# Performance work log

Hardware: AMD Instinct MI355X
Metric: run time of the kernel (lower is better)

## Reference

```python
import jax, jax.numpy as jnp
import numpy as np

N_NODES = 50000
N_EDGES = 800000
D_IN, D_HID, D_OUT = 128, 128, 64


def setup_inputs() -> dict:
    key = jax.random.key(0)
    ks = jax.random.split(key, 8)
    x = jax.random.normal(ks[0], (N_NODES, D_IN), dtype=jnp.float32)
    edge_index = jax.random.randint(ks[1], (2, N_EDGES), 0, N_NODES, dtype=jnp.int64)
    s1 = 1.0 / np.sqrt(D_IN)
    s2 = 1.0 / np.sqrt(D_HID)
    # PyG SAGEConv: out = lin_l(mean_aggr(x_j)) + lin_r(x_root); bias lives in lin_l
    Wl1 = jax.random.uniform(ks[2], (D_HID, D_IN), jnp.float32, -s1, s1)
    bl1 = jnp.zeros((D_HID,), jnp.float32)
    Wr1 = jax.random.uniform(ks[3], (D_HID, D_IN), jnp.float32, -s1, s1)
    Wl2 = jax.random.uniform(ks[4], (D_OUT, D_HID), jnp.float32, -s2, s2)
    bl2 = jnp.zeros((D_OUT,), jnp.float32)
    Wr2 = jax.random.uniform(ks[5], (D_OUT, D_HID), jnp.float32, -s2, s2)
    return {"x": x, "edge_index": edge_index, "Wl1": Wl1, "bl1": bl1, "Wr1": Wr1,
            "Wl2": Wl2, "bl2": bl2, "Wr2": Wr2}


def _sage_conv(x, src, dst, Wl, bl, Wr):
    # mean aggregation of source-node features onto destination nodes
    msg = x[src]                                              # [E, d]
    agg = jax.ops.segment_sum(msg, dst, num_segments=N_NODES)  # [N, d]
    cnt = jax.ops.segment_sum(jnp.ones((src.shape[0],), x.dtype), dst,
                              num_segments=N_NODES)            # [N]
    mean = agg / jnp.maximum(cnt, 1.0)[:, None]
    return mean @ Wl.T + bl + x @ Wr.T


def reference(x, edge_index, Wl1, bl1, Wr1, Wl2, bl2, Wr2):
    src, dst = edge_index[0], edge_index[1]
    h = jax.nn.relu(_sage_conv(x, src, dst, Wl1, bl1, Wr1))
    h = jax.nn.relu(_sage_conv(h, src, dst, Wl2, bl2, Wr2))
    return jax.nn.log_softmax(h, axis=-1)
```

## Files before the change

### kernel.cpp

```cpp
#include <hip/hip_runtime.h>
#include <cstdint>
#include <cstddef>

#define N_NODES 50000
#define N_EDGES 800000
#define ROWS_PAD 50048
#define ZROW 50000
#define BUCKET_CAP 64

#define CNT_POISON 0xAAAAAAAAu
__device__ __forceinline__ unsigned cnt_decode(unsigned raw) {
  return raw > 0x40000000u ? raw - CNT_POISON : raw;
}

typedef _Float16 f16;
typedef _Float16 f16x2 __attribute__((ext_vector_type(2)));
typedef _Float16 f16x8 __attribute__((ext_vector_type(8)));
typedef float f32x2 __attribute__((ext_vector_type(2)));
typedef float f32x4 __attribute__((ext_vector_type(4)));
typedef float fx4 __attribute__((ext_vector_type(4)));
typedef unsigned int u32x2 __attribute__((ext_vector_type(2)));
typedef unsigned short us4 __attribute__((ext_vector_type(4)));


#define NRANGE 8
#define NCHUNK 200
#define CHUNK_E (N_EDGES / NCHUNK)
#define NB_FILL (NCHUNK * NRANGE)
#define NB_CX 3125
#define NB_CW 192
#define RANGE_SZ (N_NODES / NRANGE)

__global__ __launch_bounds__(256) void preprocess_kernel(
    const int* __restrict__ edge, unsigned* __restrict__ cnt, unsigned short* __restrict__ bucket,
    const float* __restrict__ x, f16* __restrict__ X16, unsigned char* __restrict__ X8,
    unsigned char* __restrict__ H8,
    const float* __restrict__ Wl1, const float* __restrict__ Wr1,
    const float* __restrict__ Wl2, const float* __restrict__ Wr2,
    f16* __restrict__ Wc1, f16* __restrict__ Wc2) {
  const int b = blockIdx.x;
  const int tid = threadIdx.x;
  if (b < NB_FILL) {
    const int cg = b >> 6, r = (b >> 3) & 7, cl = b & 7;
    const int chunk = cg * 8 + cl;
    const int lo = r * RANGE_SZ, hi = lo + RANGE_SZ;
    const int e0 = chunk * CHUNK_E;
    #pragma unroll
    for (int i = 0; i < 16; ++i) {
      const int e = e0 + tid + i * 256;
      if (e < e0 + CHUNK_E) {
        const int dst = edge[N_EDGES + e];
        if (dst >= lo && dst < hi) {
          const int src = edge[e];
          const unsigned pos = cnt_decode(atomicAdd(&cnt[dst], 1u));
          if (pos < BUCKET_CAP) bucket[(size_t)dst * BUCKET_CAP + pos] = (unsigned short)src;
        }
      }
    }
  } else if (b < NB_FILL + NB_CX) {
    const int idx = (b - NB_FILL) * 256 + tid;
    const int row = idx >> 4, c8 = idx & 15;
    const fx4 v0 = __builtin_nontemporal_load(
        reinterpret_cast<const fx4*>(x + (size_t)row * 128 + c8 * 8));
    const fx4 v1 = __builtin_nontemporal_load(
        reinterpret_cast<const fx4*>(x + (size_t)row * 128 + c8 * 8 + 4));
    f16x8 o;
    o[0] = (f16)v0[0]; o[1] = (f16)v0[1]; o[2] = (f16)v0[2]; o[3] = (f16)v0[3];
    o[4] = (f16)v1[0]; o[5] = (f16)v1[1]; o[6] = (f16)v1[2]; o[7] = (f16)v1[3];
    *reinterpret_cast<f16x8*>(X16 + (size_t)row * 128 + c8 * 8) = o;
    u32x2 p;
    int w = __builtin_amdgcn_cvt_pk_fp8_f32(v0[0], v0[1], 0, false);
    w = __builtin_amdgcn_cvt_pk_fp8_f32(v0[2], v0[3], w, true);
    p[0] = (unsigned int)w;
    w = __builtin_amdgcn_cvt_pk_fp8_f32(v1[0], v1[1], 0, false);
    w = __builtin_amdgcn_cvt_pk_fp8_f32(v1[2], v1[3], w, true);
    p[1] = (unsigned int)w;
    *reinterpret_cast<u32x2*>(X8 + (size_t)row * 128 + c8 * 8) = p;
  } else if (b < NB_FILL + NB_CX + NB_CW) {
    const int idx = (b - NB_FILL - NB_CX) * 256 + tid;
    if (idx < 128 * 256) {
      const int n = idx >> 8, k = idx & 255;
      Wc1[idx] = (f16)((k < 128) ? Wl1[n * 128 + k] : Wr1[n * 128 + (k - 128)]);
    } else {
      const int j = idx - 128 * 256;
      const int n = j >> 8, k = j & 255;
      Wc2[j] = (f16)((k < 128) ? Wl2[n * 128 + k] : Wr2[n * 128 + (k - 128)]);
    }
  } else {
    if (tid < 32)
      reinterpret_cast<unsigned int*>(X8 + (size_t)ZROW * 128)[tid] = 0u;
    else if (tid < 64)
      reinterpret_cast<unsigned int*>(H8 + (size_t)ZROW * 128)[tid - 32] = 0u;
  }
}


__device__ __forceinline__ void aggregate_to_lds(
    const unsigned char* __restrict__ F8, const unsigned* __restrict__ cnt,
    const unsigned short* __restrict__ bucket,
    f16 (*M)[136], int wid, int lane) {
  const int quad = lane >> 4, l16 = lane & 15;
  const int nb0 = blockIdx.x * 32 + wid * 8;
  const int dv = (lane < 8) ? (int)cnt_decode(cnt[nb0 + lane]) : 0;
  us4 b4g[2];
  #pragma unroll
  for (int g = 0; g < 2; ++g)
    b4g[g] = __builtin_nontemporal_load(reinterpret_cast<const us4*>(
        bucket + (size_t)(nb0 + g * 4 + quad) * BUCKET_CAP + l16 * 4));
  const unsigned char* Fsrc = F8 + l16 * 8;
  #pragma unroll 1
  for (int g = 0; g < 2; ++g) {
    const int dq = __shfl(dv, g * 4 + quad, 64);
    const int dqc = min(dq, BUCKET_CAP);
    int md = max(max(__shfl(dv, g * 4 + 0, 64), __shfl(dv, g * 4 + 1, 64)),
                 max(__shfl(dv, g * 4 + 2, 64), __shfl(dv, g * 4 + 3, 64)));
    md = min(md, BUCKET_CAP);
    const us4 b4 = b4g[g];
    float acc[8];
    #pragma unroll
    for (int c = 0; c < 8; ++c) acc[c] = 0.f;
    for (int j = 0; j < md; j += 16) {
      u32x2 v[16];
      #pragma unroll
      for (int k = 0; k < 16; ++k) {
        const int slot = j + k;
        const int idx = __shfl((int)b4[k & 3], quad * 16 + (slot >> 2), 64);
        const int row = (slot < dqc) ? idx : ZROW;
        v[k] = *reinterpret_cast<const u32x2*>(Fsrc + (size_t)row * 128);
      }
      #pragma unroll
      for (int k = 0; k < 16; ++k) {
        const f32x2 f0 = __builtin_amdgcn_cvt_pk_f32_fp8((int)v[k][0], false);
        const f32x2 f1 = __builtin_amdgcn_cvt_pk_f32_fp8((int)v[k][0], true);
        const f32x2 f2 = __builtin_amdgcn_cvt_pk_f32_fp8((int)v[k][1], false);
        const f32x2 f3 = __builtin_amdgcn_cvt_pk_f32_fp8((int)v[k][1], true);
        acc[0] += f0[0]; acc[1] += f0[1]; acc[2] += f1[0]; acc[3] += f1[1];
        acc[4] += f2[0]; acc[5] += f2[1]; acc[6] += f3[0]; acc[7] += f3[1];
      }
    }
    const float inv = 1.0f / (float)(dq > 0 ? dq : 1);
    f16x8 o;
    #pragma unroll
    for (int c = 0; c < 8; ++c) o[c] = (f16)(acc[c] * inv);
    *reinterpret_cast<f16x8*>(&M[wid * 8 + g * 4 + quad][l16 * 8]) = o;
  }
}


__global__ __launch_bounds__(256, 4) void layer1_kernel(
    const f16* __restrict__ X16, const unsigned char* __restrict__ X8,
    const unsigned* __restrict__ cnt, const unsigned short* __restrict__ bucket,
    const f16* __restrict__ Wc, const float* __restrict__ bias,
    f16* __restrict__ H16, unsigned char* __restrict__ H8) {
  __shared__ f16 M[32][136];
  const int wid = threadIdx.x >> 6, lane = threadIdx.x & 63;
  const int quad = lane >> 4, l16 = lane & 15;
  const int rhalf = wid & 1, nhalf = wid >> 1;
  const int row0 = blockIdx.x * 32 + rhalf * 16;
  const f16* Xrow = X16 + (size_t)(row0 + l16) * 128 + quad * 8;
  f16x8 rr[4];
  #pragma unroll
  for (int s2 = 0; s2 < 4; ++s2)
    rr[s2] = __builtin_nontemporal_load(reinterpret_cast<const f16x8*>(Xrow + s2 * 32));
  aggregate_to_lds(X8, cnt, bucket, M, wid, lane);
  __syncthreads();
  f32x4 acc[4];
  #pragma unroll
  for (int t = 0; t < 4; ++t) acc[t] = (f32x4){0.f, 0.f, 0.f, 0.f};
  const f16x8* Wb = reinterpret_cast<const f16x8*>(Wc) + quad;
  #pragma unroll
  for (int s = 0; s < 8; ++s) {
    const f16x8 a = (s < 4)
        ? *reinterpret_cast<const f16x8*>(&M[rhalf * 16 + l16][quad * 8 + s * 32])
        : rr[s - 4];
    #pragma unroll
    for (int t = 0; t < 4; ++t) {
      const int u = nhalf * 4 + t;
      const f16x8 bb = Wb[(u * 16 + l16) * 32 + s * 4];
      acc[t] = __builtin_amdgcn_mfma_f32_16x16x32_f16(a, bb, acc[t], 0, 0, 0);
    }
  }
  #pragma unroll
  for (int t = 0; t < 4; ++t) {
    const int col = (nhalf * 4 + t) * 16 + l16;
    const float bv = bias[col];
    #pragma unroll
    for (int r = 0; r < 4; ++r) {
      const int row = row0 + quad * 4 + r;
      if (row < N_NODES) {
        const float vv = fmaxf(acc[t][r] + bv, 0.f);
        H16[(size_t)row * 128 + col] = (f16)vv;
        const int p = __builtin_amdgcn_cvt_pk_fp8_f32(vv, vv, 0, false);
        H8[(size_t)row * 128 + col] = (unsigned char)(p & 0xFF);
      }
    }
  }
}


__global__ __launch_bounds__(256, 4) void layer2_kernel(
    const f16* __restrict__ H16, const unsigned char* __restrict__ H8,
    const unsigned* __restrict__ cnt, const unsigned short* __restrict__ bucket,
    const f16* __restrict__ Wc, const float* __restrict__ bias,
    float* __restrict__ out) {
  __shared__ f16 M[32][136];
  __shared__ float PM[4][16], PS[4][16];
  const int wid = threadIdx.x >> 6, lane = threadIdx.x & 63;
  const int quad = lane >> 4, l16 = lane & 15;
  const int rhalf = wid & 1, nhalf = wid >> 1;
  const int row0 = blockIdx.x * 32 + rhalf * 16;
  const f16* Hrow = H16 + (size_t)(row0 + l16) * 128 + quad * 8;
  f16x8 rr[4];
  #pragma unroll
  for (int s2 = 0; s2 < 4; ++s2)
    rr[s2] = __builtin_nontemporal_load(reinterpret_cast<const f16x8*>(Hrow + s2 * 32));
  aggregate_to_lds(H8, cnt, bucket, M, wid, lane);
  __syncthreads();
  f32x4 acc[2];
  #pragma unroll
  for (int t = 0; t < 2; ++t) acc[t] = (f32x4){0.f, 0.f, 0.f, 0.f};
  const f16x8* Wb = reinterpret_cast<const f16x8*>(Wc) + quad;
  #pragma unroll
  for (int s = 0; s < 8; ++s) {
    const f16x8 a = (s < 4)
        ? *reinterpret_cast<const f16x8*>(&M[rhalf * 16 + l16][quad * 8 + s * 32])
        : rr[s - 4];
    #pragma unroll
    for (int t = 0; t < 2; ++t) {
      const int u = nhalf * 2 + t;
      const f16x8 bb = Wb[(u * 16 + l16) * 32 + s * 4];
      acc[t] = __builtin_amdgcn_mfma_f32_16x16x32_f16(a, bb, acc[t], 0, 0, 0);
    }
  }
  float bv[2];
  #pragma unroll
  for (int t = 0; t < 2; ++t) bv[t] = bias[(nhalf * 2 + t) * 16 + l16];
  float v[4][2], pm[4], ps[4];
  #pragma unroll
  for (int r = 0; r < 4; ++r) {
    #pragma unroll
    for (int t = 0; t < 2; ++t) v[r][t] = fmaxf(acc[t][r] + bv[t], 0.f);
    float m = fmaxf(v[r][0], v[r][1]);
    #pragma unroll
    for (int off = 1; off < 16; off <<= 1) m = fmaxf(m, __shfl_xor(m, off, 64));
    float s = __expf(v[r][0] - m) + __expf(v[r][1] - m);
    #pragma unroll
    for (int off = 1; off < 16; off <<= 1) s += __shfl_xor(s, off, 64);
    pm[r] = m;
    ps[r] = s;
  }
  if (l16 == 0) {
    #pragma unroll
    for (int r = 0; r < 4; ++r) {
      PM[wid][quad * 4 + r] = pm[r];
      PS[wid][quad * 4 + r] = ps[r];
    }
  }
  __syncthreads();
  #pragma unroll
  for (int r = 0; r < 4; ++r) {
    const float m2 = PM[wid ^ 2][quad * 4 + r];
    const float s2 = PS[wid ^ 2][quad * 4 + r];
    const float mt = fmaxf(pm[r], m2);
    const float st = ps[r] * __expf(pm[r] - mt) + s2 * __expf(m2 - mt);
    const float ls = mt + __logf(st);
    const int row = row0 + quad * 4 + r;
    if (row < N_NODES) {
      #pragma unroll
      for (int t = 0; t < 2; ++t)
        __builtin_nontemporal_store(
            v[r][t] - ls, out + (size_t)row * 64 + (nhalf * 2 + t) * 16 + l16);
    }
  }
}


extern "C" void kernel_launch(void* const* d_in, const int* in_sizes, int n_in,
                              void* d_out, int out_size, void* d_ws, size_t ws_size,
                              hipStream_t stream) {
  const float* x   = (const float*)d_in[0];
  const int* edge  = (const int*)d_in[1];
  const float* Wl1 = (const float*)d_in[2];
  const float* bl1 = (const float*)d_in[3];
  const float* Wr1 = (const float*)d_in[4];
  const float* Wl2 = (const float*)d_in[5];
  const float* bl2 = (const float*)d_in[6];
  const float* Wr2 = (const float*)d_in[7];
  float* out = (float*)d_out;

  char* ws = (char*)d_ws;
  size_t off = 0;
  auto alloc = [&](size_t bytes) -> char* {
    char* p = ws + off;
    off = (off + bytes + 255) & ~(size_t)255;
    return p;
  };
  unsigned* cnt          = (unsigned*)alloc((size_t)ROWS_PAD * 4);
  unsigned short* bucket = (unsigned short*)alloc((size_t)ROWS_PAD * BUCKET_CAP * 2);
  f16* X16           = (f16*)alloc((size_t)ROWS_PAD * 128 * 2);
  f16* H16           = (f16*)alloc((size_t)ROWS_PAD * 128 * 2);
  unsigned char* X8  = (unsigned char*)alloc((size_t)ROWS_PAD * 128);
  unsigned char* H8  = (unsigned char*)alloc((size_t)ROWS_PAD * 128);
  f16* Wc1           = (f16*)alloc((size_t)128 * 256 * 2);
  f16* Wc2           = (f16*)alloc((size_t)64 * 256 * 2);


  preprocess_kernel<<<NB_FILL + NB_CX + NB_CW + 1, 256, 0, stream>>>(
      edge, cnt, bucket, x, X16, X8, H8, Wl1, Wr1, Wl2, Wr2, Wc1, Wc2);

  layer1_kernel<<<ROWS_PAD / 32, 256, 0, stream>>>(X16, X8, cnt, bucket, Wc1, bl1, H16, H8);
  layer2_kernel<<<ROWS_PAD / 32, 256, 0, stream>>>(H16, H8, cnt, bucket, Wc2, bl2, out);
}
```

Before: 209.1 us.

## Software-pipeline neighbor gathers across both node groups in aggregation

Rewrites the neighbor aggregation so the two 4-node groups per wave are processed together. Gathers for the next 16-slot chunk are issued while the current chunk is decoded, so more loads are in flight and gather latency is hidden. Both groups now loop to the maximum degree over all 8 nodes instead of per group, which can add padded zero-row loads. The self-row loads are moved after the aggregation call and register use roughly doubles, which may lower occupancy.

```diff
diff --git a/kernel.cpp b/kernel.cpp
--- a/kernel.cpp
+++ b/kernel.cpp
@@ -102,48 +102,63 @@
   const int quad = lane >> 4, l16 = lane & 15;
   const int nb0 = blockIdx.x * 32 + wid * 8;
   const int dv = (lane < 8) ? (int)cnt_decode(cnt[nb0 + lane]) : 0;
-  us4 b4g[2];
-  #pragma unroll
-  for (int g = 0; g < 2; ++g)
-    b4g[g] = __builtin_nontemporal_load(reinterpret_cast<const us4*>(
-        bucket + (size_t)(nb0 + g * 4 + quad) * BUCKET_CAP + l16 * 4));
+  const us4 b40 = __builtin_nontemporal_load(reinterpret_cast<const us4*>(
+      bucket + (size_t)(nb0 + quad) * BUCKET_CAP + l16 * 4));
+  const us4 b41 = __builtin_nontemporal_load(reinterpret_cast<const us4*>(
+      bucket + (size_t)(nb0 + 4 + quad) * BUCKET_CAP + l16 * 4));
   const unsigned char* Fsrc = F8 + l16 * 8;
+  const int dq0 = __shfl(dv, quad, 64);
+  const int dq1 = __shfl(dv, 4 + quad, 64);
+  const int dqc0 = min(dq0, BUCKET_CAP), dqc1 = min(dq1, BUCKET_CAP);
+  int md = 0;
+  #pragma unroll
+  for (int n = 0; n < 8; ++n) md = max(md, __shfl(dv, n, 64));
+  md = min(md, BUCKET_CAP);
+
+  float acc0[8], acc1[8];
+  #pragma unroll
+  for (int c = 0; c < 8; ++c) { acc0[c] = 0.f; acc1[c] = 0.f; }
+  u32x2 v0[16], v1[16];
+
+#define AGG_ISSUE(vv, b4x, dqcx, jj)                                          \
+  _Pragma("unroll") for (int k = 0; k < 16; ++k) {                            \
+    const int slot = (jj) + k;  \
+    const int idx = __shfl((int)(b4x)[k & 3], quad * 16 + (slot >> 2), 64);   \
+    const int row = (slot < (dqcx)) ? idx : ZROW;    \
+    (vv)[k] = *reinterpret_cast<const u32x2*>(Fsrc + (size_t)row * 128);      \
+  }
+#define AGG_DECODE(vv, accx)                                                  \
+  _Pragma("unroll") for (int k = 0; k < 16; ++k) {                            \
+    const f32x2 f0 = __builtin_amdgcn_cvt_pk_f32_fp8((int)(vv)[k][0], false); \
+    const f32x2 f1 = __builtin_amdgcn_cvt_pk_f32_fp8((int)(vv)[k][0], true);  \
+    const f32x2 f2 = __builtin_amdgcn_cvt_pk_f32_fp8((int)(vv)[k][1], false); \
+    const f32x2 f3 = __builtin_amdgcn_cvt_pk_f32_fp8((int)(vv)[k][1], true);  \
+    (accx)[0] += f0[0]; (accx)[1] += f0[1]; (accx)[2] += f1[0]; (accx)[3] += f1[1]; \
+    (accx)[4] += f2[0]; (accx)[5] += f2[1]; (accx)[6] += f3[0]; (accx)[7] += f3[1]; \
+  }
+
+  AGG_ISSUE(v0, b40, dqc0, 0)
+  AGG_ISSUE(v1, b41, dqc1, 0)
   #pragma unroll 1
-  for (int g = 0; g < 2; ++g) {
-    const int dq = __shfl(dv, g * 4 + quad, 64);
-    const int dqc = min(dq, BUCKET_CAP);
-    int md = max(max(__shfl(dv, g * 4 + 0, 64), __shfl(dv, g * 4 + 1, 64)),
-                 max(__shfl(dv, g * 4 + 2, 64), __shfl(dv, g * 4 + 3, 64)));
-    md = min(md, BUCKET_CAP);
-    const us4 b4 = b4g[g];
-    float acc[8];
-    #pragma unroll
-    for (int c = 0; c < 8; ++c) acc[c] = 0.f;
-    for (int j = 0; j < md; j += 16) {
-      u32x2 v[16];
-      #pragma unroll
-      for (int k = 0; k < 16; ++k) {
-        const int slot = j + k;
-        const int idx = __shfl((int)b4[k & 3], quad * 16 + (slot >> 2), 64);
-        const int row = (slot < dqc) ? idx : ZROW;
-        v[k] = *reinterpret_cast<const u32x2*>(Fsrc + (size_t)row * 128);
-      }
-      #pragma unroll
-      for (int k = 0; k < 16; ++k) {
-        const f32x2 f0 = __builtin_amdgcn_cvt_pk_f32_fp8((int)v[k][0], false);
-        const f32x2 f1 = __builtin_amdgcn_cvt_pk_f32_fp8((int)v[k][0], true);
-        const f32x2 f2 = __builtin_amdgcn_cvt_pk_f32_fp8((int)v[k][1], false);
-        const f32x2 f3 = __builtin_amdgcn_cvt_pk_f32_fp8((int)v[k][1], true);
-        acc[0] += f0[0]; acc[1] += f0[1]; acc[2] += f1[0]; acc[3] += f1[1];
-        acc[4] += f2[0]; acc[5] += f2[1]; acc[6] += f3[0]; acc[7] += f3[1];
-      }
-    }
-    const float inv = 1.0f / (float)(dq > 0 ? dq : 1);
-    f16x8 o;
-    #pragma unroll
-    for (int c = 0; c < 8; ++c) o[c] = (f16)(acc[c] * inv);
-    *reinterpret_cast<f16x8*>(&M[wid * 8 + g * 4 + quad][l16 * 8]) = o;
-  }
+  for (int j = 0; j < md; j += 16) {
+    AGG_DECODE(v0, acc0)
+    if (j + 16 < md) { AGG_ISSUE(v0, b40, dqc0, j + 16) }
+    AGG_DECODE(v1, acc1)
+    if (j + 16 < md) { AGG_ISSUE(v1, b41, dqc1, j + 16) }
+  }
+#undef AGG_ISSUE
+#undef AGG_DECODE
+
+  const float inv0 = 1.0f / (float)(dq0 > 0 ? dq0 : 1);
+  const float inv1 = 1.0f / (float)(dq1 > 0 ? dq1 : 1);
+  f16x8 o0, o1;
+  #pragma unroll
+  for (int c = 0; c < 8; ++c) {
+    o0[c] = (f16)(acc0[c] * inv0);
+    o1[c] = (f16)(acc1[c] * inv1);
+  }
+  *reinterpret_cast<f16x8*>(&M[wid * 8 + quad][l16 * 8]) = o0;
+  *reinterpret_cast<f16x8*>(&M[wid * 8 + 4 + quad][l16 * 8]) = o1;
 }
 
 
@@ -157,12 +172,12 @@
   const int quad = lane >> 4, l16 = lane & 15;
   const int rhalf = wid & 1, nhalf = wid >> 1;
   const int row0 = blockIdx.x * 32 + rhalf * 16;
+  aggregate_to_lds(X8, cnt, bucket, M, wid, lane);
   const f16* Xrow = X16 + (size_t)(row0 + l16) * 128 + quad * 8;
   f16x8 rr[4];
   #pragma unroll
   for (int s2 = 0; s2 < 4; ++s2)
     rr[s2] = __builtin_nontemporal_load(reinterpret_cast<const f16x8*>(Xrow + s2 * 32));
-  aggregate_to_lds(X8, cnt, bucket, M, wid, lane);
   __syncthreads();
   f32x4 acc[4];
   #pragma unroll
@@ -209,12 +224,12 @@
   const int quad = lane >> 4, l16 = lane & 15;
   const int rhalf = wid & 1, nhalf = wid >> 1;
   const int row0 = blockIdx.x * 32 + rhalf * 16;
+  aggregate_to_lds(H8, cnt, bucket, M, wid, lane);
   const f16* Hrow = H16 + (size_t)(row0 + l16) * 128 + quad * 8;
   f16x8 rr[4];
   #pragma unroll
   for (int s2 = 0; s2 < 4; ++s2)
     rr[s2] = __builtin_nontemporal_load(reinterpret_cast<const f16x8*>(Hrow + s2 * 32));
-  aggregate_to_lds(H8, cnt, bucket, M, wid, lane);
   __syncthreads();
   f32x4 acc[2];
   #pragma unroll
```

Result: slower. 285.3 us (+36.4%).

## Split fp8 feature tables into two 64-column halves for gather locality

Applied to the files above, without the earlier changes.

Stores the fp8 node features (X8, H8) as two separate 64-byte-per-row arrays instead of one 128-byte array. The aggregation gathers each half in its own pass, with two lane groups covering alternate neighbor slots, then combines the partial sums with a cross-lane xor shuffle. Each pass touches a table half the size, which should raise cache hit rates for the random gathers. The cost is twice as many passes over the neighbor list and an extra shuffle reduction.

```diff
diff --git a/kernel.cpp b/kernel.cpp
--- a/kernel.cpp
+++ b/kernel.cpp
@@ -14,7 +14,6 @@
 }
 
 typedef _Float16 f16;
-typedef _Float16 f16x2 __attribute__((ext_vector_type(2)));
 typedef _Float16 f16x8 __attribute__((ext_vector_type(8)));
 typedef float f32x2 __attribute__((ext_vector_type(2)));
 typedef float f32x4 __attribute__((ext_vector_type(4)));
@@ -33,8 +32,9 @@
 
 __global__ __launch_bounds__(256) void preprocess_kernel(
     const int* __restrict__ edge, unsigned* __restrict__ cnt, unsigned short* __restrict__ bucket,
-    const float* __restrict__ x, f16* __restrict__ X16, unsigned char* __restrict__ X8,
-    unsigned char* __restrict__ H8,
+    const float* __restrict__ x, f16* __restrict__ X16,
+    unsigned char* __restrict__ X8a, unsigned char* __restrict__ X8b,
+    unsigned char* __restrict__ H8a, unsigned char* __restrict__ H8b,
     const float* __restrict__ Wl1, const float* __restrict__ Wr1,
     const float* __restrict__ Wl2, const float* __restrict__ Wr2,
     f16* __restrict__ Wc1, f16* __restrict__ Wc2) {
@@ -75,7 +75,9 @@
     w = __builtin_amdgcn_cvt_pk_fp8_f32(v1[0], v1[1], 0, false);
     w = __builtin_amdgcn_cvt_pk_fp8_f32(v1[2], v1[3], w, true);
     p[1] = (unsigned int)w;
-    *reinterpret_cast<u32x2*>(X8 + (size_t)row * 128 + c8 * 8) = p;
+    unsigned char* dst8 = (c8 < 8) ? (X8a + (size_t)row * 64 + c8 * 8)
+                                   : (X8b + (size_t)row * 64 + (c8 - 8) * 8);
+    *reinterpret_cast<u32x2*>(dst8) = p;
   } else if (b < NB_FILL + NB_CX + NB_CW) {
     const int idx = (b - NB_FILL - NB_CX) * 256 + tid;
     if (idx < 128 * 256) {
@@ -87,19 +89,24 @@
       Wc2[j] = (f16)((k < 128) ? Wl2[n * 128 + k] : Wr2[n * 128 + (k - 128)]);
     }
   } else {
-    if (tid < 32)
-      reinterpret_cast<unsigned int*>(X8 + (size_t)ZROW * 128)[tid] = 0u;
+    if (tid < 16)
+      reinterpret_cast<unsigned int*>(X8a + (size_t)ZROW * 64)[tid] = 0u;
+    else if (tid < 32)
+      reinterpret_cast<unsigned int*>(X8b + (size_t)ZROW * 64)[tid - 16] = 0u;
+    else if (tid < 48)
+      reinterpret_cast<unsigned int*>(H8a + (size_t)ZROW * 64)[tid - 32] = 0u;
     else if (tid < 64)
-      reinterpret_cast<unsigned int*>(H8 + (size_t)ZROW * 128)[tid - 32] = 0u;
+      reinterpret_cast<unsigned int*>(H8b + (size_t)ZROW * 64)[tid - 48] = 0u;
   }
 }
 
 
 __device__ __forceinline__ void aggregate_to_lds(
-    const unsigned char* __restrict__ F8, const unsigned* __restrict__ cnt,
-    const unsigned short* __restrict__ bucket,
+    const unsigned char* __restrict__ F8a, const unsigned char* __restrict__ F8b,
+    const unsigned* __restrict__ cnt, const unsigned short* __restrict__ bucket,
     f16 (*M)[136], int wid, int lane) {
   const int quad = lane >> 4, l16 = lane & 15;
+  const int half8 = l16 >> 3, l8 = l16 & 7;
   const int nb0 = blockIdx.x * 32 + wid * 8;
   const int dv = (lane < 8) ? (int)cnt_decode(cnt[nb0 + lane]) : 0;
   us4 b4g[2];
@@ -107,7 +114,6 @@
   for (int g = 0; g < 2; ++g)
     b4g[g] = __builtin_nontemporal_load(reinterpret_cast<const us4*>(
         bucket + (size_t)(nb0 + g * 4 + quad) * BUCKET_CAP + l16 * 4));
-  const unsigned char* Fsrc = F8 + l16 * 8;
   #pragma unroll 1
   for (int g = 0; g < 2; ++g) {
     const int dq = __shfl(dv, g * 4 + quad, 64);
@@ -116,42 +122,51 @@
                  max(__shfl(dv, g * 4 + 2, 64), __shfl(dv, g * 4 + 3, 64)));
     md = min(md, BUCKET_CAP);
     const us4 b4 = b4g[g];
-    float acc[8];
-    #pragma unroll
-    for (int c = 0; c < 8; ++c) acc[c] = 0.f;
-    for (int j = 0; j < md; j += 16) {
-      u32x2 v[16];
+    const float inv = 1.0f / (float)(dq > 0 ? dq : 1);
+    #pragma unroll 1
+    for (int p = 0; p < 2; ++p) {
+      const unsigned char* Fsrc = (p == 0 ? F8a : F8b) + l8 * 8;
+      float acc[8];
       #pragma unroll
-      for (int k = 0; k < 16; ++k) {
-        const int slot = j + k;
-        const int idx = __shfl((int)b4[k & 3], quad * 16 + (slot >> 2), 64);
-        const int row = (slot < dqc) ? idx : ZROW;
-        v[k] = *reinterpret_cast<const u32x2*>(Fsrc + (size_t)row * 128);
+      for (int c = 0; c < 8; ++c) acc[c] = 0.f;
+      for (int j = 0; j < md; j += 32) {
+        u32x2 v[16];
+        #pragma unroll
+        for (int k = 0; k < 16; ++k) {
+          const int slot = j + k + half8 * 16;
+          const int idx = __shfl((int)b4[k & 3],
+                                 quad * 16 + ((j + k) >> 2) + half8 * 4, 64);
+          const int row = (slot < dqc) ? idx : ZROW;
+          v[k] = *reinterpret_cast<const u32x2*>(Fsrc + (size_t)row * 64);
+        }
+        #pragma unroll
+        for (int k = 0; k < 16; ++k) {
+          const f32x2 f0 = __builtin_amdgcn_cvt_pk_f32_fp8((int)v[k][0], false);
+          const f32x2 f1 = __builtin_amdgcn_cvt_pk_f32_fp8((int)v[k][0], true);
+          const f32x2 f2 = __builtin_amdgcn_cvt_pk_f32_fp8((int)v[k][1], false);
+          const f32x2 f3 = __builtin_amdgcn_cvt_pk_f32_fp8((int)v[k][1], true);
+          acc[0] += f0[0]; acc[1] += f0[1]; acc[2] += f1[0]; acc[3] += f1[1];
+          acc[4] += f2[0]; acc[5] += f2[1]; acc[6] += f3[0]; acc[7] += f3[1];
+        }
       }
       #pragma unroll
-      for (int k = 0; k < 16; ++k) {
-        const f32x2 f0 = __builtin_amdgcn_cvt_pk_f32_fp8((int)v[k][0], false);
-        const f32x2 f1 = __builtin_amdgcn_cvt_pk_f32_fp8((int)v[k][0], true);
-        const f32x2 f2 = __builtin_amdgcn_cvt_pk_f32_fp8((int)v[k][1], false);
-        const f32x2 f3 = __builtin_amdgcn_cvt_pk_f32_fp8((int)v[k][1], true);
-        acc[0] += f0[0]; acc[1] += f0[1]; acc[2] += f1[0]; acc[3] += f1[1];
-        acc[4] += f2[0]; acc[5] += f2[1]; acc[6] += f3[0]; acc[7] += f3[1];
-      }
-    }
-    const float inv = 1.0f / (float)(dq > 0 ? dq : 1);
-    f16x8 o;
-    #pragma unroll
-    for (int c = 0; c < 8; ++c) o[c] = (f16)(acc[c] * inv);
-    *reinterpret_cast<f16x8*>(&M[wid * 8 + g * 4 + quad][l16 * 8]) = o;
+      for (int c = 0; c < 8; ++c) acc[c] += __shfl_xor(acc[c], 8, 64);
+      f16x8 o;
+      #pragma unroll
+      for (int c = 0; c < 8; ++c) o[c] = (f16)(acc[c] * inv);
+      *reinterpret_cast<f16x8*>(&M[wid * 8 + g * 4 + quad][p * 64 + l8 * 8]) = o;
+    }
   }
 }
 
 
 __global__ __launch_bounds__(256, 4) void layer1_kernel(
-    const f16* __restrict__ X16, const unsigned char* __restrict__ X8,
+    const f16* __restrict__ X16,
+    const unsigned char* __restrict__ X8a, const unsigned char* __restrict__ X8b,
     const unsigned* __restrict__ cnt, const unsigned short* __restrict__ bucket,
     const f16* __restrict__ Wc, const float* __restrict__ bias,
-    f16* __restrict__ H16, unsigned char* __restrict__ H8) {
+    f16* __restrict__ H16,
+    unsigned char* __restrict__ H8a, unsigned char* __restrict__ H8b) {
   __shared__ f16 M[32][136];
   const int wid = threadIdx.x >> 6, lane = threadIdx.x & 63;
   const int quad = lane >> 4, l16 = lane & 15;
@@ -162,7 +177,7 @@
   #pragma unroll
   for (int s2 = 0; s2 < 4; ++s2)
     rr[s2] = __builtin_nontemporal_load(reinterpret_cast<const f16x8*>(Xrow + s2 * 32));
-  aggregate_to_lds(X8, cnt, bucket, M, wid, lane);
+  aggregate_to_lds(X8a, X8b, cnt, bucket, M, wid, lane);
   __syncthreads();
   f32x4 acc[4];
   #pragma unroll
@@ -182,8 +197,11 @@
   }
   #pragma unroll
   for (int t = 0; t < 4; ++t) {
-    const int col = (nhalf * 4 + t) * 16 + l16;
+    const int u = nhalf * 4 + t;
+    const int col = u * 16 + l16;
     const float bv = bias[col];
+    unsigned char* H8t = (u < 4) ? H8a : H8b;
+    const int colh = col & 63;
     #pragma unroll
     for (int r = 0; r < 4; ++r) {
       const int row = row0 + quad * 4 + r;
@@ -191,7 +209,7 @@
         const float vv = fmaxf(acc[t][r] + bv, 0.f);
         H16[(size_t)row * 128 + col] = (f16)vv;
         const int p = __builtin_amdgcn_cvt_pk_fp8_f32(vv, vv, 0, false);
-        H8[(size_t)row * 128 + col] = (unsigned char)(p & 0xFF);
+        H8t[(size_t)row * 64 + colh] = (unsigned char)(p & 0xFF);
       }
     }
   }
@@ -199,7 +217,8 @@
 
 
 __global__ __launch_bounds__(256, 4) void layer2_kernel(
-    const f16* __restrict__ H16, const unsigned char* __restrict__ H8,
+    const f16* __restrict__ H16,
+    const unsigned char* __restrict__ H8a, const unsigned char* __restrict__ H8b,
     const unsigned* __restrict__ cnt, const unsigned short* __restrict__ bucket,
     const f16* __restrict__ Wc, const float* __restrict__ bias,
     float* __restrict__ out) {
@@ -214,7 +233,7 @@
   #pragma unroll
   for (int s2 = 0; s2 < 4; ++s2)
     rr[s2] = __builtin_nontemporal_load(reinterpret_cast<const f16x8*>(Hrow + s2 * 32));
-  aggregate_to_lds(H8, cnt, bucket, M, wid, lane);
+  aggregate_to_lds(H8a, H8b, cnt, bucket, M, wid, lane);
   __syncthreads();
   f32x4 acc[2];
   #pragma unroll
@@ -299,15 +318,19 @@
   unsigned short* bucket = (unsigned short*)alloc((size_t)ROWS_PAD * BUCKET_CAP * 2);
   f16* X16           = (f16*)alloc((size_t)ROWS_PAD * 128 * 2);
   f16* H16           = (f16*)alloc((size_t)ROWS_PAD * 128 * 2);
-  unsigned char* X8  = (unsigned char*)alloc((size_t)ROWS_PAD * 128);
-  unsigned char* H8  = (unsigned char*)alloc((size_t)ROWS_PAD * 128);
+  unsigned char* X8a = (unsigned char*)alloc((size_t)ROWS_PAD * 64);
+  unsigned char* X8b = (unsigned char*)alloc((size_t)ROWS_PAD * 64);
+  unsigned char* H8a = (unsigned char*)alloc((size_t)ROWS_PAD * 64);
+  unsigned char* H8b = (unsigned char*)alloc((size_t)ROWS_PAD * 64);
   f16* Wc1           = (f16*)alloc((size_t)128 * 256 * 2);
   f16* Wc2           = (f16*)alloc((size_t)64 * 256 * 2);
 
 
   preprocess_kernel<<<NB_FILL + NB_CX + NB_CW + 1, 256, 0, stream>>>(
-      edge, cnt, bucket, x, X16, X8, H8, Wl1, Wr1, Wl2, Wr2, Wc1, Wc2);
-
-  layer1_kernel<<<ROWS_PAD / 32, 256, 0, stream>>>(X16, X8, cnt, bucket, Wc1, bl1, H16, H8);
-  layer2_kernel<<<ROWS_PAD / 32, 256, 0, stream>>>(H16, H8, cnt, bucket, Wc2, bl2, out);
-}
+      edge, cnt, bucket, x, X16, X8a, X8b, H8a, H8b, Wl1, Wr1, Wl2, Wr2, Wc1, Wc2);
+
+  layer1_kernel<<<ROWS_PAD / 32, 256, 0, stream>>>(
+      X16, X8a, X8b, cnt, bucket, Wc1, bl1, H16, H8a, H8b);
+  layer2_kernel<<<ROWS_PAD / 32, 256, 0, stream>>>(
+      H16, H8a, H8b, cnt, bucket, Wc2, bl2, out);
+}
```

After: 210.9 us. About the same (+0.9%).

## Apply layer-2 linear transforms before aggregation to shrink gathered features

Applied to the files above, without the earlier changes.

Uses the linearity of mean aggregation to compute H·Wl2ᵀ and H·Wr2ᵀ inside the layer-1 kernel, which adds a second MFMA stage on the hidden tile held in LDS. Layer 2 then gathers 64-wide FP8 projected rows instead of 128-wide hidden rows, and its GEMM is replaced by an add, bias, ReLU and log-softmax. This halves the gather traffic of the second aggregation and removes the H16/H8 round trip. In exchange layer 1 does more compute, and quantising the projected values to FP8 changes the numerical error profile.

```diff
diff --git a/kernel.cpp b/kernel.cpp
--- a/kernel.cpp
+++ b/kernel.cpp
@@ -14,7 +14,6 @@
 }
 
 typedef _Float16 f16;
-typedef _Float16 f16x2 __attribute__((ext_vector_type(2)));
 typedef _Float16 f16x8 __attribute__((ext_vector_type(8)));
 typedef float f32x2 __attribute__((ext_vector_type(2)));
 typedef float f32x4 __attribute__((ext_vector_type(4)));
@@ -34,10 +33,10 @@
 __global__ __launch_bounds__(256) void preprocess_kernel(
     const int* __restrict__ edge, unsigned* __restrict__ cnt, unsigned short* __restrict__ bucket,
     const float* __restrict__ x, f16* __restrict__ X16, unsigned char* __restrict__ X8,
-    unsigned char* __restrict__ H8,
+    unsigned char* __restrict__ Hp8,
     const float* __restrict__ Wl1, const float* __restrict__ Wr1,
     const float* __restrict__ Wl2, const float* __restrict__ Wr2,
-    f16* __restrict__ Wc1, f16* __restrict__ Wc2) {
+    f16* __restrict__ Wc1, f16* __restrict__ Wc2p) {
   const int b = blockIdx.x;
   const int tid = threadIdx.x;
   if (b < NB_FILL) {
@@ -83,14 +82,14 @@
       Wc1[idx] = (f16)((k < 128) ? Wl1[n * 128 + k] : Wr1[n * 128 + (k - 128)]);
     } else {
       const int j = idx - 128 * 256;
-      const int n = j >> 8, k = j & 255;
-      Wc2[j] = (f16)((k < 128) ? Wl2[n * 128 + k] : Wr2[n * 128 + (k - 128)]);
+      const int n = j >> 7, k = j & 127;
+      Wc2p[j] = (f16)((n < 64) ? Wl2[n * 128 + k] : Wr2[(n - 64) * 128 + k]);
     }
   } else {
     if (tid < 32)
       reinterpret_cast<unsigned int*>(X8 + (size_t)ZROW * 128)[tid] = 0u;
-    else if (tid < 64)
-      reinterpret_cast<unsigned int*>(H8 + (size_t)ZROW * 128)[tid - 32] = 0u;
+    else if (tid < 48)
+      reinterpret_cast<unsigned int*>(Hp8 + (size_t)ZROW * 64)[tid - 32] = 0u;
   }
 }
 
@@ -151,8 +150,10 @@
     const f16* __restrict__ X16, const unsigned char* __restrict__ X8,
     const unsigned* __restrict__ cnt, const unsigned short* __restrict__ bucket,
     const f16* __restrict__ Wc, const float* __restrict__ bias,
-    f16* __restrict__ H16, unsigned char* __restrict__ H8) {
+    const f16* __restrict__ Wc2p,
+    unsigned char* __restrict__ Hp8, f16* __restrict__ R2f) {
   __shared__ f16 M[32][136];
+  __shared__ f16 HT[32][136];
   const int wid = threadIdx.x >> 6, lane = threadIdx.x & 63;
   const int quad = lane >> 4, l16 = lane & 15;
   const int rhalf = wid & 1, nhalf = wid >> 1;
@@ -186,12 +187,40 @@
     const float bv = bias[col];
     #pragma unroll
     for (int r = 0; r < 4; ++r) {
+      const int rl = rhalf * 16 + quad * 4 + r;
+      HT[rl][col] = (f16)fmaxf(acc[t][r] + bv, 0.f);
+    }
+  }
+  __syncthreads();
+  f32x4 acc2[4];
+  #pragma unroll
+  for (int t = 0; t < 4; ++t) acc2[t] = (f32x4){0.f, 0.f, 0.f, 0.f};
+  const f16x8* Wb2 = reinterpret_cast<const f16x8*>(Wc2p) + quad;
+  #pragma unroll
+  for (int s = 0; s < 4; ++s) {
+    const f16x8 a2 = *reinterpret_cast<const f16x8*>(&HT[rhalf * 16 + l16][quad * 8 + s * 32]);
+    #pragma unroll
+    for (int t = 0; t < 4; ++t) {
+      const int u = nhalf * 4 + t;
+      const f16x8 bb = Wb2[(u * 16 + l16) * 16 + s * 4];
+      acc2[t] = __builtin_amdgcn_mfma_f32_16x16x32_f16(a2, bb, acc2[t], 0, 0, 0);
+    }
+  }
+  #pragma unroll
+  for (int t = 0; t < 4; ++t) {
+    const int u = nhalf * 4 + t;
+    const int col2 = u * 16 + l16;
+    #pragma unroll
+    for (int r = 0; r < 4; ++r) {
       const int row = row0 + quad * 4 + r;
       if (row < N_NODES) {
-        const float vv = fmaxf(acc[t][r] + bv, 0.f);
-        H16[(size_t)row * 128 + col] = (f16)vv;
-        const int p = __builtin_amdgcn_cvt_pk_fp8_f32(vv, vv, 0, false);
-        H8[(size_t)row * 128 + col] = (unsigned char)(p & 0xFF);
+        const float vv = acc2[t][r];
+        if (u < 4) {
+          const int p = __builtin_amdgcn_cvt_pk_fp8_f32(vv, vv, 0, false);
+          Hp8[(size_t)row * 64 + col2] = (unsigned char)(p & 0xFF);
+        } else {
+          R2f[(size_t)row * 64 + (col2 - 64)] = (f16)vv;
+        }
       }
     }
   }
@@ -199,78 +228,92 @@
 
 
 __global__ __launch_bounds__(256, 4) void layer2_kernel(
-    const f16* __restrict__ H16, const unsigned char* __restrict__ H8,
+    const unsigned char* __restrict__ Hp8, const f16* __restrict__ R2f,
     const unsigned* __restrict__ cnt, const unsigned short* __restrict__ bucket,
-    const f16* __restrict__ Wc, const float* __restrict__ bias,
-    float* __restrict__ out) {
-  __shared__ f16 M[32][136];
-  __shared__ float PM[4][16], PS[4][16];
+    const float* __restrict__ bias, float* __restrict__ out) {
+  __shared__ f16 M2[32][72];
   const int wid = threadIdx.x >> 6, lane = threadIdx.x & 63;
   const int quad = lane >> 4, l16 = lane & 15;
-  const int rhalf = wid & 1, nhalf = wid >> 1;
-  const int row0 = blockIdx.x * 32 + rhalf * 16;
-  const f16* Hrow = H16 + (size_t)(row0 + l16) * 128 + quad * 8;
-  f16x8 rr[4];
-  #pragma unroll
-  for (int s2 = 0; s2 < 4; ++s2)
-    rr[s2] = __builtin_nontemporal_load(reinterpret_cast<const f16x8*>(Hrow + s2 * 32));
-  aggregate_to_lds(H8, cnt, bucket, M, wid, lane);
+  const int half8 = l16 >> 3, l8 = l16 & 7;
+  const int nb0 = blockIdx.x * 32 + wid * 8;
+  const int dv = (lane < 8) ? (int)cnt_decode(cnt[nb0 + lane]) : 0;
+  us4 b4g[2];
+  #pragma unroll
+  for (int g = 0; g < 2; ++g)
+    b4g[g] = __builtin_nontemporal_load(reinterpret_cast<const us4*>(
+        bucket + (size_t)(nb0 + g * 4 + quad) * BUCKET_CAP + l16 * 4));
+  const unsigned char* Fsrc = Hp8 + l8 * 8;
+  #pragma unroll 1
+  for (int g = 0; g < 2; ++g) {
+    const int dq = __shfl(dv, g * 4 + quad, 64);
+    const int dqc = min(dq, BUCKET_CAP);
+    int md = max(max(__shfl(dv, g * 4 + 0, 64), __shfl(dv, g * 4 + 1, 64)),
+                 max(__shfl(dv, g * 4 + 2, 64), __shfl(dv, g * 4 + 3, 64)));
+    md = min(md, BUCKET_CAP);
+    const us4 b4 = b4g[g];
+    float acc[8];
+    #pragma unroll
+    for (int c = 0; c < 8; ++c) acc[c] = 0.f;
+    for (int j = 0; j < md; j += 32) {
+      u32x2 v[16];
+      #pragma unroll
+      for (int k = 0; k < 16; ++k) {
+        const int slot = j + k + half8 * 16;
+        const int idx = __shfl((int)b4[k & 3],
+                               quad * 16 + ((j + k) >> 2) + half8 * 4, 64);
+        const int row = (slot < dqc) ? idx : ZROW;
+        v[k] = *reinterpret_cast<const u32x2*>(Fsrc + (size_t)row * 64);
+      }
+      #pragma unroll
+      for (int k = 0; k < 16; ++k) {
+        const f32x2 f0 = __builtin_amdgcn_cvt_pk_f32_fp8((int)v[k][0], false);
+        const f32x2 f1 = __builtin_amdgcn_cvt_pk_f32_fp8((int)v[k][0], true);
+        const f32x2 f2 = __builtin_amdgcn_cvt_pk_f32_fp8((int)v[k][1], false);
+        const f32x2 f3 = __builtin_amdgcn_cvt_pk_f32_fp8((int)v[k][1], true);
+        acc[0] += f0[0]; acc[1] += f0[1]; acc[2] += f1[0]; acc[3] += f1[1];
+        acc[4] += f2[0]; acc[5] += f2[1]; acc[6] += f3[0]; acc[7] += f3[1];
+      }
+    }
+    #pragma unroll
+    for (int c = 0; c < 8; ++c) acc[c] += __shfl_xor(acc[c], 8, 64);
+    const float inv = 1.0f / (float)(dq > 0 ? dq : 1);
+    f16x8 o;
+    #pragma unroll
+    for (int c = 0; c < 8; ++c) o[c] = (f16)(acc[c] * inv);
+    *reinterpret_cast<f16x8*>(&M2[wid * 8 + g * 4 + quad][l8 * 8]) = o;
+  }
   __syncthreads();
-  f32x4 acc[2];
-  #pragma unroll
-  for (int t = 0; t < 2; ++t) acc[t] = (f32x4){0.f, 0.f, 0.f, 0.f};
-  const f16x8* Wb = reinterpret_cast<const f16x8*>(Wc) + quad;
-  #pragma unroll
-  for (int s = 0; s < 8; ++s) {
-    const f16x8 a = (s < 4)
-        ? *reinterpret_cast<const f16x8*>(&M[rhalf * 16 + l16][quad * 8 + s * 32])
-        : rr[s - 4];
-    #pragma unroll
-    for (int t = 0; t < 2; ++t) {
-      const int u = nhalf * 2 + t;
-      const f16x8 bb = Wb[(u * 16 + l16) * 32 + s * 4];
-      acc[t] = __builtin_amdgcn_mfma_f32_16x16x32_f16(a, bb, acc[t], 0, 0, 0);
-    }
-  }
-  float bv[2];
-  #pragma unroll
-  for (int t = 0; t < 2; ++t) bv[t] = bias[(nhalf * 2 + t) * 16 + l16];
-  float v[4][2], pm[4], ps[4];
-  #pragma unroll
-  for (int r = 0; r < 4; ++r) {
-    #pragma unroll
-    for (int t = 0; t < 2; ++t) v[r][t] = fmaxf(acc[t][r] + bv[t], 0.f);
-    float m = fmaxf(v[r][0], v[r][1]);
-    #pragma unroll
-    for (int off = 1; off < 16; off <<= 1) m = fmaxf(m, __shfl_xor(m, off, 64));
-    float s = __expf(v[r][0] - m) + __expf(v[r][1] - m);
-    #pragma unroll
-    for (int off = 1; off < 16; off <<= 1) s += __shfl_xor(s, off, 64);
-    pm[r] = m;
-    ps[r] = s;
-  }
-  if (l16 == 0) {
-    #pragma unroll
-    for (int r = 0; r < 4; ++r) {
-      PM[wid][quad * 4 + r] = pm[r];
-      PS[wid][quad * 4 + r] = ps[r];
-    }
-  }
-  __syncthreads();
-  #pragma unroll
-  for (int r = 0; r < 4; ++r) {
-    const float m2 = PM[wid ^ 2][quad * 4 + r];
-    const float s2 = PS[wid ^ 2][quad * 4 + r];
-    const float mt = fmaxf(pm[r], m2);
-    const float st = ps[r] * __expf(pm[r] - mt) + s2 * __expf(m2 - mt);
-    const float ls = mt + __logf(st);
-    const int row = row0 + quad * 4 + r;
-    if (row < N_NODES) {
-      #pragma unroll
-      for (int t = 0; t < 2; ++t)
-        __builtin_nontemporal_store(
-            v[r][t] - ls, out + (size_t)row * 64 + (nhalf * 2 + t) * 16 + l16);
-    }
+  const int rl = wid * 8 + (lane >> 3);
+  const int row = blockIdx.x * 32 + rl;
+  const f16x8 mv = *reinterpret_cast<const f16x8*>(&M2[rl][l8 * 8]);
+  f16x8 r2v = {};
+  if (row < N_NODES)
+    r2v = *reinterpret_cast<const f16x8*>(R2f + (size_t)row * 64 + l8 * 8);
+  const fx4 b0 = *reinterpret_cast<const fx4*>(bias + l8 * 8);
+  const fx4 b1 = *reinterpret_cast<const fx4*>(bias + l8 * 8 + 4);
+  float v[8];
+  #pragma unroll
+  for (int c = 0; c < 8; ++c) {
+    const float bb = (c < 4) ? b0[c] : b1[c - 4];
+    v[c] = fmaxf((float)mv[c] + (float)r2v[c] + bb, 0.f);
+  }
+  float m = v[0];
+  #pragma unroll
+  for (int c = 1; c < 8; ++c) m = fmaxf(m, v[c]);
+  #pragma unroll
+  for (int off = 1; off < 8; off <<= 1) m = fmaxf(m, __shfl_xor(m, off, 64));
+  float s = 0.f;
+  #pragma unroll
+  for (int c = 0; c < 8; ++c) s += __expf(v[c] - m);
+  #pragma unroll
+  for (int off = 1; off < 8; off <<= 1) s += __shfl_xor(s, off, 64);
+  const float ls = m + __logf(s);
+  if (row < N_NODES) {
+    fx4 o0, o1;
+    #pragma unroll
+    for (int c = 0; c < 4; ++c) { o0[c] = v[c] - ls; o1[c] = v[c + 4] - ls; }
+    __builtin_nontemporal_store(o0, reinterpret_cast<fx4*>(out + (size_t)row * 64 + l8 * 8));
+    __builtin_nontemporal_store(o1, reinterpret_cast<fx4*>(out + (size_t)row * 64 + l8 * 8 + 4));
   }
 }
 
@@ -298,16 +341,18 @@
   unsigned* cnt          = (unsigned*)alloc((size_t)ROWS_PAD * 4);
   unsigned short* bucket = (unsigned short*)alloc((size_t)ROWS_PAD * BUCKET_CAP * 2);
   f16* X16           = (f16*)alloc((size_t)ROWS_PAD * 128 * 2);
-  f16* H16           = (f16*)alloc((size_t)ROWS_PAD * 128 * 2);
   unsigned char* X8  = (unsigned char*)alloc((size_t)ROWS_PAD * 128);
-  unsigned char* H8  = (unsigned char*)alloc((size_t)ROWS_PAD * 128);
+  unsigned char* Hp8 = (unsigned char*)alloc((size_t)ROWS_PAD * 64);
+  f16* R2f           = (f16*)alloc((size_t)ROWS_PAD * 64 * 2);
   f16* Wc1           = (f16*)alloc((size_t)128 * 256 * 2);
-  f16* Wc2           = (f16*)alloc((size_t)64 * 256 * 2);
+  f16* Wc2p          = (f16*)alloc((size_t)128 * 128 * 2);
 
 
   preprocess_kernel<<<NB_FILL + NB_CX + NB_CW + 1, 256, 0, stream>>>(
-      edge, cnt, bucket, x, X16, X8, H8, Wl1, Wr1, Wl2, Wr2, Wc1, Wc2);
-
-  layer1_kernel<<<ROWS_PAD / 32, 256, 0, stream>>>(X16, X8, cnt, bucket, Wc1, bl1, H16, H8);
-  layer2_kernel<<<ROWS_PAD / 32, 256, 0, stream>>>(H16, H8, cnt, bucket, Wc2, bl2, out);
-}
+      edge, cnt, bucket, x, X16, X8, Hp8, Wl1, Wr1, Wl2, Wr2, Wc1, Wc2p);
+
+  layer1_kernel<<<ROWS_PAD / 32, 256, 0, stream>>>(
+      X16, X8, cnt, bucket, Wc1, bl1, Wc2p, Hp8, R2f);
+  layer2_kernel<<<ROWS_PAD / 32, 256, 0, stream>>>(
+      Hp8, R2f, cnt, bucket, bl2, out);
+}
```

Measured after the change: 198.7 us. 5.0% less time.
